# Performance work log

Measured on AMD Instinct MI355X. Metric: run time of the kernel, lower is better.

Reference implementation:

```python
import jax, jax.numpy as jnp
import numpy as np

N = 100000      # nodes
E = 1600000     # edges (unique, no self-loops)
DIN = 128
DOUT = 128


def _make_edges():
    """Unique undirected edges, no self-loops, ring guarantees min degree 2.
    Ensures dense-adjacency semantics == edge-list segment-sum semantics."""
    rng = np.random.default_rng(0)
    ring = np.stack([np.arange(N, dtype=np.int64), (np.arange(N, dtype=np.int64) + 1) % N], axis=1)
    ring = np.sort(ring, axis=1)  # canonical (min,max)
    ring_keys = ring[:, 0] * N + ring[:, 1]
    cand = rng.integers(0, N, size=(3 * E, 2), dtype=np.int64)
    cand = cand[cand[:, 0] != cand[:, 1]]
    cand = np.sort(cand, axis=1)
    keys = cand[:, 0] * N + cand[:, 1]
    _, idx = np.unique(keys, return_index=True)
    cand = cand[np.sort(idx)]
    cand = cand[~np.isin(cand[:, 0] * N + cand[:, 1], ring_keys)][: E - N]
    edges = np.concatenate([ring, cand], axis=0)  # [E, 2]
    return edges.T  # [2, E]


def setup_inputs() -> dict:
    key = jax.random.key(0)
    kx, kw = jax.random.split(key)
    X = jax.random.normal(kx, (N, DIN), dtype=jnp.float32)
    # kaiming_normal_ default (fan_in mode): std = sqrt(2 / fan_in)
    W = jax.random.normal(kw, (DIN, DOUT), dtype=jnp.float32) * np.float32(np.sqrt(2.0 / DIN))
    edge_list = jnp.asarray(_make_edges(), dtype=jnp.int64)
    return {"X": X, "W": W, "edge_list": edge_list}


def reference(X, W, edge_list):
    src, dst = edge_list[0], edge_list[1]
    n = X.shape[0]
    ones = jnp.ones(src.shape[0], dtype=X.dtype)
    # D: each edge increments both endpoint degrees (matches the torch loop)
    deg = jnp.zeros((n,), X.dtype).at[src].add(ones).at[dst].add(ones)
    # A_hat @ X = symmetric neighbor aggregation + self (identity)
    agg = jnp.zeros_like(X).at[dst].add(X[src]).at[src].add(X[dst]) + X
    # D^-1 is inverse of diagonal -> elementwise reciprocal
    z = (agg / deg[:, None]) @ W
    return jax.nn.relu(z)
```

## Files before the change

### kernel.cpp

```cpp
#include <hip/hip_runtime.h>


#define DFEAT 128
#define BSH 7
#define BNODES (1 << BSH)
#define NBMAX 800
#define EPB 8192
#define SORT_CAP 6144

typedef __attribute__((ext_vector_type(8))) short short8;
typedef __attribute__((ext_vector_type(4))) float f32x4;

__device__ __forceinline__ unsigned short f2bf(float x) {
  unsigned u = __float_as_uint(x);
  return (unsigned short)((u + 0x7FFFu + ((u >> 16) & 1u)) >> 16);
}
__device__ __forceinline__ float bf2f(unsigned short h) {
  return __uint_as_float((unsigned)h << 16);
}

__global__ void zero_kernel(int* p, int n) {
  int i = blockIdx.x * blockDim.x + threadIdx.x;
  if (i < n) p[i] = 0;
}

__global__ void detect_kernel(const int* el32, int* flag) {
  if (threadIdx.x == 0 && blockIdx.x == 0)
    flag[0] = (el32[1] == 0 && el32[3] == 0) ? 1 : 0;
}

__device__ __forceinline__ int edge_at(const void* el, long long i, int mode64) {
  if (mode64) return (int)((const long long*)el)[i];
  return ((const int*)el)[i];
}

__global__ __launch_bounds__(1024) void hist_kernel(const void* el,
                                                    const int* __restrict__ flag,
                                                    int* __restrict__ ghist,
                                                    int E, int NB) {
  __shared__ int lh[NBMAX];
  int t = threadIdx.x;
  for (int i = t; i < NB; i += 1024) lh[i] = 0;
  __syncthreads();
  int m = flag[0];
  long long e0 = (long long)blockIdx.x * EPB + t;
#pragma unroll
  for (int r = 0; r < 8; r++) {
    long long e = e0 + r * 1024;
    if (e < E) {
      int s = edge_at(el, e, m);
      int d = edge_at(el, (long long)E + e, m);
      atomicAdd(&lh[s >> BSH], 1);
      atomicAdd(&lh[d >> BSH], 1);
    }
  }
  __syncthreads();
  for (int i = t; i < NB; i += 1024)
    if (lh[i]) atomicAdd(&ghist[i], lh[i]);
}

__global__ __launch_bounds__(1024) void scan_kernel(const int* __restrict__ ghist,
                                                    int* __restrict__ gbase,
                                                    int* __restrict__ gcur, int NB) {
  __shared__ int s[1024];
  int t = threadIdx.x;
  int v = (t < NB) ? ghist[t] : 0;
  s[t] = v;
  __syncthreads();
  for (int d = 1; d < 1024; d <<= 1) {
    int a = (t >= d) ? s[t - d] : 0;
    __syncthreads();
    s[t] += a;
    __syncthreads();
  }
  if (t < NB) {
    int ex = s[t] - v;
    gbase[t] = ex;
    gcur[t] = ex;
  }
}

__global__ __launch_bounds__(1024) void scatter_kernel(const void* el,
                                                       const int* __restrict__ flag,
                                                       int* __restrict__ gcur,
                                                       unsigned int* __restrict__ bucket,
                                                       int E, int NB) {
  __shared__ int lh[NBMAX];
  __shared__ int lb[NBMAX];
  int t = threadIdx.x;
  for (int i = t; i < NB; i += 1024) lh[i] = 0;
  __syncthreads();
  int m = flag[0];
  long long e0 = (long long)blockIdx.x * EPB + t;
  int s[8], d[8];
#pragma unroll
  for (int r = 0; r < 8; r++) {
    long long e = e0 + r * 1024;
    if (e < E) {
      s[r] = edge_at(el, e, m);
      d[r] = edge_at(el, (long long)E + e, m);
    } else {
      s[r] = -1;
    }
  }
#pragma unroll
  for (int r = 0; r < 8; r++) {
    if (s[r] >= 0) {
      atomicAdd(&lh[s[r] >> BSH], 1);
      atomicAdd(&lh[d[r] >> BSH], 1);
    }
  }
  __syncthreads();
  for (int i = t; i < NB; i += 1024) {
    int c = lh[i];
    lb[i] = c ? atomicAdd(&gcur[i], c) : 0;
  }
  __syncthreads();
  for (int i = t; i < NB; i += 1024) lh[i] = 0;
  __syncthreads();
#pragma unroll
  for (int r = 0; r < 8; r++) {
    if (s[r] >= 0) {
      int bs = s[r] >> BSH, bd = d[r] >> BSH;
      int ps = lb[bs] + atomicAdd(&lh[bs], 1);
      bucket[ps] = ((unsigned)(s[r] & (BNODES - 1)) << 20) | (unsigned)d[r];
      int pd = lb[bd] + atomicAdd(&lh[bd], 1);
      bucket[pd] = ((unsigned)(d[r] & (BNODES - 1)) << 20) | (unsigned)s[r];
    }
  }
}

__global__ __launch_bounds__(1024) void sort_kernel(const unsigned int* __restrict__ bucket,
                                                    const int* __restrict__ gbase,
                                                    const int* __restrict__ ghist,
                                                    int* __restrict__ adj,
                                                    int* __restrict__ off,
                                                    int n, int NB) {
  __shared__ unsigned ent[SORT_CAP];
  __shared__ int srt[SORT_CAP];
  __shared__ int h[BNODES];
  __shared__ int pref[BNODES];
  __shared__ int cur[BNODES];
  int b = blockIdx.x, t = threadIdx.x;
  int base = gbase[b], cnt = ghist[b];
  if (cnt > SORT_CAP) cnt = SORT_CAP;
  if (t < BNODES) h[t] = 0;
  __syncthreads();
  for (int i = t; i < cnt; i += 1024) {
    unsigned e = bucket[base + i];
    ent[i] = e;
    atomicAdd(&h[e >> 20], 1);
  }
  __syncthreads();
  if (t == 0) {
    int s = 0;
    for (int i = 0; i < BNODES; i++) { pref[i] = s; s += h[i]; }
  }
  __syncthreads();
  if (t < BNODES) cur[t] = pref[t];
  __syncthreads();
  for (int i = t; i < cnt; i += 1024) {
    unsigned e = ent[i];
    int p = atomicAdd(&cur[e >> 20], 1);
    srt[p] = (int)(e & 0xFFFFFu);
  }
  __syncthreads();
  for (int i = t; i < cnt; i += 1024) adj[base + i] = srt[i];
  int node0 = b << BSH;
  if (t < BNODES && node0 + t < n) off[node0 + t] = base + pref[t];
  if (t == 0 && b == NB - 1) off[n] = base + cnt;
}

__global__ __launch_bounds__(256) void wfrag_kernel(const float* __restrict__ W,
                                                    unsigned int* __restrict__ Wfrag) {
  int e = blockIdx.x * 256 + threadIdx.x;
  if (e >= 2048) return;
  int lane = e & 63;
  int nt = (e >> 6) & 7;
  int kc = e >> 9;
  int k0 = kc * 32 + (lane >> 4) * 8;
  int col = nt * 16 + (lane & 15);
  unsigned int o[4];
#pragma unroll
  for (int jj = 0; jj < 4; jj++) {
    unsigned short lo = f2bf(W[(k0 + 2 * jj) * DFEAT + col]);
    unsigned short hi = f2bf(W[(k0 + 2 * jj + 1) * DFEAT + col]);
    o[jj] = (unsigned)lo | ((unsigned)hi << 16);
  }
  uint4* dst = (uint4*)Wfrag;
  uint4 v; v.x = o[0]; v.y = o[1]; v.z = o[2]; v.w = o[3];
  dst[e] = v;
}

__global__ __launch_bounds__(256) void gemm_kernel(const float* __restrict__ X,
                                                   const short8* __restrict__ Wfrag,
                                                   unsigned short* __restrict__ Yb, int n) {
  int wave = threadIdx.x >> 6;
  int lane = threadIdx.x & 63;
  int row0 = (blockIdx.x * 4 + wave) * 16;
  if (row0 >= n) return;

  int rowA = row0 + (lane & 15);
  if (rowA >= n) rowA = n - 1;
  const float4* Xrow = (const float4*)(X + (long long)rowA * DFEAT);
  int koff = (lane >> 4) * 2;

  f32x4 acc[8];
#pragma unroll
  for (int ntp = 0; ntp < 8; ntp++) acc[ntp] = (f32x4){0.f, 0.f, 0.f, 0.f};

#pragma unroll
  for (int kc = 0; kc < 4; kc++) {
    float4 xa = Xrow[kc * 8 + koff];
    float4 xb = Xrow[kc * 8 + koff + 1];
    short8 a8;
    a8[0] = (short)f2bf(xa.x); a8[1] = (short)f2bf(xa.y);
    a8[2] = (short)f2bf(xa.z); a8[3] = (short)f2bf(xa.w);
    a8[4] = (short)f2bf(xb.x); a8[5] = (short)f2bf(xb.y);
    a8[6] = (short)f2bf(xb.z); a8[7] = (short)f2bf(xb.w);
#pragma unroll
    for (int nt = 0; nt < 8; nt++) {
      short8 b8 = Wfrag[(kc * 8 + nt) * 64 + lane];
      acc[nt] = __builtin_amdgcn_mfma_f32_16x16x32_bf16(a8, b8, acc[nt], 0, 0, 0);
    }
  }

  int rbase = row0 + (lane >> 4) * 4;
  int cbase = lane & 15;
#pragma unroll
  for (int nt = 0; nt < 8; nt++) {
#pragma unroll
    for (int r = 0; r < 4; r++) {
      int row = rbase + r;
      if (row < n)
        Yb[(long long)row * DFEAT + nt * 16 + cbase] = f2bf(acc[nt][r]);
    }
  }
}

__global__ __launch_bounds__(256) void gather_kernel(const ushort2* __restrict__ Yb,
                                                     const int* __restrict__ off,
                                                     const int* __restrict__ adj,
                                                     float2* __restrict__ out2, int n) {
  int wid = (int)((blockIdx.x * (long long)blockDim.x + threadIdx.x) >> 6);
  int lane = threadIdx.x & 63;
  if (wid >= n) return;

  int off0 = off[wid], off1 = off[wid + 1];
  ushort2 sf = Yb[(long long)wid * 64 + lane];
  float ax = bf2f(sf.x), ay = bf2f(sf.y);

  for (int base = off0; base < off1; base += 64) {
    int cnt = off1 - base; if (cnt > 64) cnt = 64;
    int idx = (lane < cnt) ? adj[base + lane] : 0;
    int t = 0;
    for (; t + 8 <= cnt; t += 8) {
      ushort2 v[8];
#pragma unroll
      for (int u = 0; u < 8; u++) {
        int j = __shfl(idx, t + u);
        v[u] = Yb[(long long)j * 64 + lane];
      }
#pragma unroll
      for (int u = 0; u < 8; u++) {
        ax += bf2f(v[u].x);
        ay += bf2f(v[u].y);
      }
    }
    for (; t < cnt; t++) {
      int j = __shfl(idx, t);
      ushort2 v = Yb[(long long)j * 64 + lane];
      ax += bf2f(v.x);
      ay += bf2f(v.y);
    }
  }

  float invd = 1.0f / (float)(off1 - off0);
  ax *= invd; ay *= invd;
  float2 o;
  o.x = ax > 0.f ? ax : 0.f;
  o.y = ay > 0.f ? ay : 0.f;
  out2[(long long)wid * 64 + lane] = o;
}

extern "C" void kernel_launch(void* const* d_in, const int* in_sizes, int n_in,
                              void* d_out, int out_size, void* d_ws, size_t ws_size,
                              hipStream_t stream) {
  const float* X = (const float*)d_in[0];
  const float* W = (const float*)d_in[1];
  const void* el = d_in[2];
  float* out = (float*)d_out;

  int n = in_sizes[0] / DFEAT;
  int E = in_sizes[2] / 2;
  int NB = (n + BNODES - 1) >> BSH;

  char* p = (char*)d_ws;
  auto alloc = [&](size_t bytes) -> char* {
    char* q = p;
    p += (bytes + 511) & ~(size_t)511;
    return q;
  };
  int* ghist = (int*)alloc((size_t)NBMAX * 4);
  int* gbase = (int*)alloc((size_t)NBMAX * 4);
  int* gcur  = (int*)alloc((size_t)NBMAX * 4);
  int* flag  = (int*)alloc(64);
  unsigned int* bucket = (unsigned int*)alloc((size_t)2 * E * 4);
  int* adj   = (int*)alloc((size_t)2 * E * 4);
  int* off   = (int*)alloc((size_t)(n + 1) * 4);
  unsigned int* Wfrag = (unsigned int*)alloc((size_t)2048 * 16);
  unsigned short* Yb = (unsigned short*)alloc((size_t)n * DFEAT * 2);

  int eblocks = (E + EPB - 1) / EPB;

  detect_kernel<<<1, 64, 0, stream>>>((const int*)el, flag);
  zero_kernel<<<(NB + 255) / 256, 256, 0, stream>>>(ghist, NB);
  hist_kernel<<<eblocks, 1024, 0, stream>>>(el, flag, ghist, E, NB);
  scan_kernel<<<1, 1024, 0, stream>>>(ghist, gbase, gcur, NB);
  scatter_kernel<<<eblocks, 1024, 0, stream>>>(el, flag, gcur, bucket, E, NB);
  sort_kernel<<<NB, 1024, 0, stream>>>(bucket, gbase, ghist, adj, off, n, NB);
  wfrag_kernel<<<8, 256, 0, stream>>>(W, Wfrag);
  gemm_kernel<<<(n + 63) / 64, 256, 0, stream>>>(X, (const short8*)Wfrag, Yb, n);
  gather_kernel<<<(n + 3) / 4, 256, 0, stream>>>((const ushort2*)Yb, off, adj,
                                                 (float2*)out, n);
}
```

Before: 286.2 us.

## Fuse bucket sort into gather, drop histogram pass, use fp16 packed accumulation

```diff
diff --git a/kernel.cpp b/kernel.cpp
--- a/kernel.cpp
+++ b/kernel.cpp
@@ -1,4 +1,5 @@
 #include <hip/hip_runtime.h>
+#include <hip/hip_fp16.h>
 
 
 #define DFEAT 128
@@ -15,69 +16,19 @@
   unsigned u = __float_as_uint(x);
   return (unsigned short)((u + 0x7FFFu + ((u >> 16) & 1u)) >> 16);
 }
-__device__ __forceinline__ float bf2f(unsigned short h) {
-  return __uint_as_float((unsigned)h << 16);
-}
-
-__global__ void zero_kernel(int* p, int n) {
+__device__ __forceinline__ __half2 u2h(unsigned x) {
+  union { unsigned u; __half2 h; } c; c.u = x; return c.h;
+}
+
+__global__ void init_kernel(const int* el32, int* gcur, int* flag, int NB) {
   int i = blockIdx.x * blockDim.x + threadIdx.x;
-  if (i < n) p[i] = 0;
-}
-
-__global__ void detect_kernel(const int* el32, int* flag) {
-  if (threadIdx.x == 0 && blockIdx.x == 0)
-    flag[0] = (el32[1] == 0 && el32[3] == 0) ? 1 : 0;
+  if (i < NB) gcur[i] = 0;
+  if (i == 0) flag[0] = (el32[1] == 0 && el32[3] == 0) ? 1 : 0;
 }
 
 __device__ __forceinline__ int edge_at(const void* el, long long i, int mode64) {
   if (mode64) return (int)((const long long*)el)[i];
   return ((const int*)el)[i];
-}
-
-__global__ __launch_bounds__(1024) void hist_kernel(const void* el,
-                                                    const int* __restrict__ flag,
-                                                    int* __restrict__ ghist,
-                                                    int E, int NB) {
-  __shared__ int lh[NBMAX];
-  int t = threadIdx.x;
-  for (int i = t; i < NB; i += 1024) lh[i] = 0;
-  __syncthreads();
-  int m = flag[0];
-  long long e0 = (long long)blockIdx.x * EPB + t;
-#pragma unroll
-  for (int r = 0; r < 8; r++) {
-    long long e = e0 + r * 1024;
-    if (e < E) {
-      int s = edge_at(el, e, m);
-      int d = edge_at(el, (long long)E + e, m);
-      atomicAdd(&lh[s >> BSH], 1);
-      atomicAdd(&lh[d >> BSH], 1);
-    }
-  }
-  __syncthreads();
-  for (int i = t; i < NB; i += 1024)
-    if (lh[i]) atomicAdd(&ghist[i], lh[i]);
-}
-
-__global__ __launch_bounds__(1024) void scan_kernel(const int* __restrict__ ghist,
-                                                    int* __restrict__ gbase,
-                                                    int* __restrict__ gcur, int NB) {
-  __shared__ int s[1024];
-  int t = threadIdx.x;
-  int v = (t < NB) ? ghist[t] : 0;
-  s[t] = v;
-  __syncthreads();
-  for (int d = 1; d < 1024; d <<= 1) {
-    int a = (t >= d) ? s[t - d] : 0;
-    __syncthreads();
-    s[t] += a;
-    __syncthreads();
-  }
-  if (t < NB) {
-    int ex = s[t] - v;
-    gbase[t] = ex;
-    gcur[t] = ex;
-  }
 }
 
 __global__ __launch_bounds__(1024) void scatter_kernel(const void* el,
@@ -123,52 +74,15 @@
     if (s[r] >= 0) {
       int bs = s[r] >> BSH, bd = d[r] >> BSH;
       int ps = lb[bs] + atomicAdd(&lh[bs], 1);
-      bucket[ps] = ((unsigned)(s[r] & (BNODES - 1)) << 20) | (unsigned)d[r];
+      if (ps < SORT_CAP)
+        bucket[(long long)bs * SORT_CAP + ps] =
+            ((unsigned)(s[r] & (BNODES - 1)) << 20) | (unsigned)d[r];
       int pd = lb[bd] + atomicAdd(&lh[bd], 1);
-      bucket[pd] = ((unsigned)(d[r] & (BNODES - 1)) << 20) | (unsigned)s[r];
-    }
-  }
-}
-
-__global__ __launch_bounds__(1024) void sort_kernel(const unsigned int* __restrict__ bucket,
-                                                    const int* __restrict__ gbase,
-                                                    const int* __restrict__ ghist,
-                                                    int* __restrict__ adj,
-                                                    int* __restrict__ off,
-                                                    int n, int NB) {
-  __shared__ unsigned ent[SORT_CAP];
-  __shared__ int srt[SORT_CAP];
-  __shared__ int h[BNODES];
-  __shared__ int pref[BNODES];
-  __shared__ int cur[BNODES];
-  int b = blockIdx.x, t = threadIdx.x;
-  int base = gbase[b], cnt = ghist[b];
-  if (cnt > SORT_CAP) cnt = SORT_CAP;
-  if (t < BNODES) h[t] = 0;
-  __syncthreads();
-  for (int i = t; i < cnt; i += 1024) {
-    unsigned e = bucket[base + i];
-    ent[i] = e;
-    atomicAdd(&h[e >> 20], 1);
-  }
-  __syncthreads();
-  if (t == 0) {
-    int s = 0;
-    for (int i = 0; i < BNODES; i++) { pref[i] = s; s += h[i]; }
-  }
-  __syncthreads();
-  if (t < BNODES) cur[t] = pref[t];
-  __syncthreads();
-  for (int i = t; i < cnt; i += 1024) {
-    unsigned e = ent[i];
-    int p = atomicAdd(&cur[e >> 20], 1);
-    srt[p] = (int)(e & 0xFFFFFu);
-  }
-  __syncthreads();
-  for (int i = t; i < cnt; i += 1024) adj[base + i] = srt[i];
-  int node0 = b << BSH;
-  if (t < BNODES && node0 + t < n) off[node0 + t] = base + pref[t];
-  if (t == 0 && b == NB - 1) off[n] = base + cnt;
+      if (pd < SORT_CAP)
+        bucket[(long long)bd * SORT_CAP + pd] =
+            ((unsigned)(d[r] & (BNODES - 1)) << 20) | (unsigned)s[r];
+    }
+  }
 }
 
 __global__ __launch_bounds__(256) void wfrag_kernel(const float* __restrict__ W,
@@ -194,7 +108,7 @@
 
 __global__ __launch_bounds__(256) void gemm_kernel(const float* __restrict__ X,
                                                    const short8* __restrict__ Wfrag,
-                                                   unsigned short* __restrict__ Yb, int n) {
+                                                   __half* __restrict__ Yh, int n) {
   int wave = threadIdx.x >> 6;
   int lane = threadIdx.x & 63;
   int row0 = (blockIdx.x * 4 + wave) * 16;
@@ -233,54 +147,100 @@
     for (int r = 0; r < 4; r++) {
       int row = rbase + r;
       if (row < n)
-        Yb[(long long)row * DFEAT + nt * 16 + cbase] = f2bf(acc[nt][r]);
-    }
-  }
-}
-
-__global__ __launch_bounds__(256) void gather_kernel(const ushort2* __restrict__ Yb,
-                                                     const int* __restrict__ off,
-                                                     const int* __restrict__ adj,
-                                                     float2* __restrict__ out2, int n) {
-  int wid = (int)((blockIdx.x * (long long)blockDim.x + threadIdx.x) >> 6);
-  int lane = threadIdx.x & 63;
-  if (wid >= n) return;
-
-  int off0 = off[wid], off1 = off[wid + 1];
-  ushort2 sf = Yb[(long long)wid * 64 + lane];
-  float ax = bf2f(sf.x), ay = bf2f(sf.y);
-
-  for (int base = off0; base < off1; base += 64) {
-    int cnt = off1 - base; if (cnt > 64) cnt = 64;
-    int idx = (lane < cnt) ? adj[base + lane] : 0;
-    int t = 0;
-    for (; t + 8 <= cnt; t += 8) {
-      ushort2 v[8];
-#pragma unroll
-      for (int u = 0; u < 8; u++) {
-        int j = __shfl(idx, t + u);
-        v[u] = Yb[(long long)j * 64 + lane];
-      }
-#pragma unroll
-      for (int u = 0; u < 8; u++) {
-        ax += bf2f(v[u].x);
-        ay += bf2f(v[u].y);
-      }
-    }
-    for (; t < cnt; t++) {
-      int j = __shfl(idx, t);
-      ushort2 v = Yb[(long long)j * 64 + lane];
-      ax += bf2f(v.x);
-      ay += bf2f(v.y);
-    }
-  }
-
-  float invd = 1.0f / (float)(off1 - off0);
-  ax *= invd; ay *= invd;
-  float2 o;
-  o.x = ax > 0.f ? ax : 0.f;
-  o.y = ay > 0.f ? ay : 0.f;
-  out2[(long long)wid * 64 + lane] = o;
+        Yh[(long long)row * DFEAT + nt * 16 + cbase] = __float2half(acc[nt][r]);
+    }
+  }
+}
+
+__global__ __launch_bounds__(1024, 8) void gather_kernel(const __half* __restrict__ Yh,
+                                                         const int* __restrict__ gcur,
+                                                         const unsigned int* __restrict__ bucket,
+                                                         float* __restrict__ out, int n) {
+  __shared__ unsigned int srt[SORT_CAP];
+  __shared__ int h[BNODES], pref[BNODES], cur[BNODES], scn[BNODES];
+  int b = blockIdx.x, t = threadIdx.x;
+  int cnt = gcur[b]; if (cnt > SORT_CAP) cnt = SORT_CAP;
+  long long base = (long long)b * SORT_CAP;
+
+  if (t < BNODES) h[t] = 0;
+  __syncthreads();
+  for (int i = t; i < cnt; i += 1024)
+    atomicAdd(&h[bucket[base + i] >> 20], 1);
+  __syncthreads();
+  int v = (t < BNODES) ? h[t] : 0;
+  if (t < BNODES) scn[t] = v;
+  __syncthreads();
+  for (int dd = 1; dd < BNODES; dd <<= 1) {
+    int a = (t < BNODES && t >= dd) ? scn[t - dd] : 0;
+    __syncthreads();
+    if (t < BNODES) scn[t] += a;
+    __syncthreads();
+  }
+  if (t < BNODES) { pref[t] = scn[t] - v; cur[t] = scn[t] - v; }
+  __syncthreads();
+  for (int i = t; i < cnt; i += 1024) {
+    unsigned e = bucket[base + i];
+    int p = atomicAdd(&cur[e >> 20], 1);
+    srt[p] = e & 0xFFFFFu;
+  }
+  __syncthreads();
+
+  int wv = t >> 6, lane = t & 63;
+  int sub = lane >> 4, fl = lane & 15;
+  const uint4* Y4 = (const uint4*)Yh;
+
+  for (int oo = 0; oo < 8; oo++) {
+    int o = wv * 8 + oo;
+    int node = (b << BSH) + o;
+    if (node >= n) break;
+    int start = pref[o], len = h[o];
+
+    __half2 a0 = u2h(0), a1 = u2h(0), a2 = u2h(0), a3 = u2h(0);
+    if (sub == 0) {
+      uint4 u = Y4[(long long)node * 16 + fl];
+      a0 = __hadd2(a0, u2h(u.x)); a1 = __hadd2(a1, u2h(u.y));
+      a2 = __hadd2(a2, u2h(u.z)); a3 = __hadd2(a3, u2h(u.w));
+    }
+    int i = sub;
+    for (; i + 4 < len; i += 8) {
+      unsigned j0 = srt[start + i];
+      unsigned j1 = srt[start + i + 4];
+      uint4 u0 = Y4[(long long)j0 * 16 + fl];
+      uint4 u1 = Y4[(long long)j1 * 16 + fl];
+      a0 = __hadd2(a0, u2h(u0.x)); a1 = __hadd2(a1, u2h(u0.y));
+      a2 = __hadd2(a2, u2h(u0.z)); a3 = __hadd2(a3, u2h(u0.w));
+      a0 = __hadd2(a0, u2h(u1.x)); a1 = __hadd2(a1, u2h(u1.y));
+      a2 = __hadd2(a2, u2h(u1.z)); a3 = __hadd2(a3, u2h(u1.w));
+    }
+    if (i < len) {
+      unsigned j0 = srt[start + i];
+      uint4 u0 = Y4[(long long)j0 * 16 + fl];
+      a0 = __hadd2(a0, u2h(u0.x)); a1 = __hadd2(a1, u2h(u0.y));
+      a2 = __hadd2(a2, u2h(u0.z)); a3 = __hadd2(a3, u2h(u0.w));
+    }
+
+    float2 f0 = __half22float2(a0), f1 = __half22float2(a1);
+    float2 f2 = __half22float2(a2), f3 = __half22float2(a3);
+    float g[8] = {f0.x, f0.y, f1.x, f1.y, f2.x, f2.y, f3.x, f3.y};
+#pragma unroll
+    for (int k = 0; k < 8; k++) {
+      g[k] += __shfl_xor(g[k], 16);
+      g[k] += __shfl_xor(g[k], 32);
+    }
+    if (sub == 0) {
+      float inv = 1.0f / (float)len;
+      float4 o0, o1;
+      o0.x = g[0] * inv; o0.y = g[1] * inv; o0.z = g[2] * inv; o0.w = g[3] * inv;
+      o1.x = g[4] * inv; o1.y = g[5] * inv; o1.z = g[6] * inv; o1.w = g[7] * inv;
+      o0.x = o0.x > 0.f ? o0.x : 0.f; o0.y = o0.y > 0.f ? o0.y : 0.f;
+      o0.z = o0.z > 0.f ? o0.z : 0.f; o0.w = o0.w > 0.f ? o0.w : 0.f;
+      o1.x = o1.x > 0.f ? o1.x : 0.f; o1.y = o1.y > 0.f ? o1.y : 0.f;
+      o1.z = o1.z > 0.f ? o1.z : 0.f; o1.w = o1.w > 0.f ? o1.w : 0.f;
+      float4* op = (float4*)(out + (long long)node * DFEAT);
+      op[fl * 2] = o0;
+      op[fl * 2 + 1] = o1;
+    }
+  }
 }
 
 extern "C" void kernel_launch(void* const* d_in, const int* in_sizes, int n_in,
@@ -301,26 +261,17 @@
     p += (bytes + 511) & ~(size_t)511;
     return q;
   };
-  int* ghist = (int*)alloc((size_t)NBMAX * 4);
-  int* gbase = (int*)alloc((size_t)NBMAX * 4);
-  int* gcur  = (int*)alloc((size_t)NBMAX * 4);
-  int* flag  = (int*)alloc(64);
-  unsigned int* bucket = (unsigned int*)alloc((size_t)2 * E * 4);
-  int* adj   = (int*)alloc((size_t)2 * E * 4);
-  int* off   = (int*)alloc((size_t)(n + 1) * 4);
+  int* gcur = (int*)alloc((size_t)NBMAX * 4);
+  int* flag = (int*)alloc(64);
+  unsigned int* bucket = (unsigned int*)alloc((size_t)NBMAX * SORT_CAP * 4);
   unsigned int* Wfrag = (unsigned int*)alloc((size_t)2048 * 16);
-  unsigned short* Yb = (unsigned short*)alloc((size_t)n * DFEAT * 2);
+  __half* Yh = (__half*)alloc((size_t)n * DFEAT * 2);
 
   int eblocks = (E + EPB - 1) / EPB;
 
-  detect_kernel<<<1, 64, 0, stream>>>((const int*)el, flag);
-  zero_kernel<<<(NB + 255) / 256, 256, 0, stream>>>(ghist, NB);
-  hist_kernel<<<eblocks, 1024, 0, stream>>>(el, flag, ghist, E, NB);
-  scan_kernel<<<1, 1024, 0, stream>>>(ghist, gbase, gcur, NB);
+  init_kernel<<<(NBMAX + 255) / 256, 256, 0, stream>>>((const int*)el, gcur, flag, NB);
   scatter_kernel<<<eblocks, 1024, 0, stream>>>(el, flag, gcur, bucket, E, NB);
-  sort_kernel<<<NB, 1024, 0, stream>>>(bucket, gbase, ghist, adj, off, n, NB);
   wfrag_kernel<<<8, 256, 0, stream>>>(W, Wfrag);
-  gemm_kernel<<<(n + 63) / 64, 256, 0, stream>>>(X, (const short8*)Wfrag, Yb, n);
-  gather_kernel<<<(n + 3) / 4, 256, 0, stream>>>((const ushort2*)Yb, off, adj,
-                                                 (float2*)out, n);
-}
+  gemm_kernel<<<(n + 63) / 64, 256, 0, stream>>>(X, (const short8*)Wfrag, Yh, n);
+  gather_kernel<<<NB, 1024, 0, stream>>>(Yh, gcur, bucket, out, n);
+}
```

Measured after the change: 273.0 us. -4.6%, faster.
